# Performance work log

Measured on AMD Instinct MI355X. Metric: run time of the kernel, lower is better.

## Reference

```python
import jax, jax.numpy as jnp
import numpy as np

# Conv / geometry config (matches init_kwargs)
CIN, COUT = 16, 32
H, W = 16, 16
KH, KW = 3, 3
STRIDE, PAD = 1, 1
OH = (H + 2 * PAD - KH) // STRIDE + 1
OW = (W + 2 * PAD - KW) // STRIDE + 1
IN_DIM = CIN * H * W      # 4096
OUT_DIM = COUT * OH * OW  # 8192
N = 256                   # number of constraint rows


def full_toeplitz(weight):
    """Dense Toeplitz matrix T [Cout*Oh*Ow, Cin*H*W] with conv(x) = T @ x.flatten().

    out[co,oh,ow] = sum_{ci,kh,kw} w[co,ci,kh,kw] * x[ci, oh*s+kh-p, ow*s+kw-p].
    So T entry at (co,oh,ow),(ci,ih,iw) = w[co,ci, ih-(oh*s-p), iw-(ow*s-p)] if in-range.
    """
    dt = weight.dtype
    oh = jnp.arange(OH)
    ih = jnp.arange(H)
    kh = ih[None, :] - (oh[:, None] * STRIDE - PAD)          # [Oh, H]
    mh = ((kh >= 0) & (kh < KH)).astype(dt)
    khc = jnp.clip(kh, 0, KH - 1)
    ow = jnp.arange(OW)
    iw = jnp.arange(W)
    kw = iw[None, :] - (ow[:, None] * STRIDE - PAD)          # [Ow, W]
    mw = ((kw >= 0) & (kw < KW)).astype(dt)
    kwc = jnp.clip(kw, 0, KW - 1)
    # gather kernel rows: [Cout, Cin, Oh, H, Kw]
    g1 = weight[:, :, khc, :] * mh[None, None, :, :, None]
    # gather kernel cols: [Cout, Cin, Oh, H, Ow, W]
    g2 = g1[..., kwc] * mw[None, None, None, None, :, :]
    T = g2.transpose(0, 2, 4, 1, 3, 5).reshape(OUT_DIM, IN_DIM)
    return T


def setup_inputs() -> dict:
    key = jax.random.key(0)
    ks = jax.random.split(key, 6)
    return {
        "uc": jax.random.normal(ks[0], (N, OUT_DIM), dtype=jnp.float32),
        "lc": jax.random.normal(ks[1], (N, OUT_DIM), dtype=jnp.float32),
        "uc_bias": jax.random.normal(ks[2], (N,), dtype=jnp.float32),
        "lc_bias": jax.random.normal(ks[3], (N,), dtype=jnp.float32),
        "weight": jax.random.normal(ks[4], (COUT, CIN, KH, KW), dtype=jnp.float32),
        "bias": jax.random.normal(ks[5], (COUT,), dtype=jnp.float32),
    }


def reference(uc, lc, uc_bias, lc_bias, weight, bias):
    # VerifyConv2d._init_linear: Toeplitz weights + repeat_interleave'd bias,
    # then VerifyLinear.backsubstitute: dense GEMMs.
    T = full_toeplitz(weight)                      # [out_dim, in_dim]
    bvec = jnp.repeat(bias, OH * OW)               # [out_dim]
    new_uc_bias = uc_bias + uc @ bvec              # [N]
    new_lc_bias = lc_bias + lc @ bvec              # [N]
    new_uc = uc @ T                                # [N, in_dim]
    new_lc = lc @ T                                # [N, in_dim]
    return new_uc, new_lc, new_uc_bias, new_lc_bias
```

## Files before the change

kernel.cpp:

```cpp
#include <hip/hip_runtime.h>


#define NROWS   256
#define OUT_CH  32
#define IN_CH   16
#define SPAT    256
#define IN_DIM  4096
#define OUT_DIM 8192
#define CO_STRIDE 289

typedef __attribute__((ext_vector_type(8))) short    bf16x8;
typedef __attribute__((ext_vector_type(4))) float    f32x4;
typedef __attribute__((ext_vector_type(4))) unsigned u32x4;

__global__ __launch_bounds__(256) void backsub(
    const float* __restrict__ uc, const float* __restrict__ lc,
    const float* __restrict__ ucb, const float* __restrict__ lcb,
    const float* __restrict__ w, const float* __restrict__ bias,
    float* __restrict__ out)
{
    __shared__ float act[OUT_CH * CO_STRIDE];
    __shared__ unsigned short bfr16[9 * 2 * 512];
    __shared__ float red[4];

    const int t     = threadIdx.x;
    const int n     = blockIdx.x & 255;
    const int which = blockIdx.x >> 8;

    for (int i = t; i < OUT_CH * 16 * 2; i += 256) {
        int co = i >> 5, rr = i & 31, row = rr >> 1, side = rr & 1;
        act[co * CO_STRIDE + row * 18 + side * 17] = 0.f;
    }

    #pragma unroll
    for (int i = 0; i < 18; ++i) {
        int v = t + i * 256;
        int j = v >> 9, rem = v & 511, co = rem >> 4, ci = rem & 15;
        float wv = w[(co * IN_CH + ci) * 9 + j];
        unsigned hb = __float_as_uint(wv) & 0xffff0000u;
        float    lf = wv - __uint_as_float(hb);
        unsigned lb = __float_as_uint(lf) & 0xffff0000u;
        int lane = ((co >> 3) << 4) | ci;
        int r    = co & 7;
        bfr16[(2 * j + 0) * 512 + lane * 8 + r] = (unsigned short)(hb >> 16);
        bfr16[(2 * j + 1) * 512 + lane * 8 + r] = (unsigned short)(lb >> 16);
    }

    const float*  srow = (which ? lc : uc) + (size_t)n * OUT_DIM;
    const float4* s4   = (const float4*)srow;
    float bs = 0.f;
    #pragma unroll
    for (int k = 0; k < 8; ++k) {
        float4 f = s4[t + k * 256];
        int co  = (t >> 6) + 4 * k;
        bs += bias[co] * (f.x + f.y + f.z + f.w);
        int ih  = (t >> 2) & 15;
        int iw0 = (t & 3) * 4;
        int wd  = co * CO_STRIDE + ih * 18 + 1 + iw0;
        act[wd + 0] = f.x; act[wd + 1] = f.y; act[wd + 2] = f.z; act[wd + 3] = f.w;
    }
    #pragma unroll
    for (int o = 32; o > 0; o >>= 1) bs += __shfl_down(bs, o, 64);
    if ((t & 63) == 0) red[t >> 6] = bs;

    __syncthreads();

    if (t == 0) {
        const float* cb = which ? lcb : ucb;
        out[2 * (size_t)NROWS * IN_DIM + which * NROWS + n] =
            cb[n] + red[0] + red[1] + red[2] + red[3];
    }

    const int l    = t & 63;
    const int wave = t >> 6;
    const int co_g = l >> 4;
    const int il   = l & 15;

    bf16x8 Bh[9], Bl[9];
    #pragma unroll
    for (int j = 0; j < 9; ++j) {
        Bh[j] = *(const bf16x8*)&bfr16[(2 * j + 0) * 512 + l * 8];
        Bl[j] = *(const bf16x8*)&bfr16[(2 * j + 1) * 512 + l * 8];
    }

    f32x4 acc[4];
    #pragma unroll
    for (int mt = 0; mt < 4; ++mt) acc[mt] = (f32x4){0.f, 0.f, 0.f, 0.f};

    #pragma unroll
    for (int mt = 0; mt < 4; ++mt) {
        const int ih = wave * 4 + mt;
        #pragma unroll
        for (int j = 0; j < 9; ++j) {
            const int kh = j / 3, kw = j % 3;
            const int ihn = ih + 1 - kh;
            if ((unsigned)ihn < 16u) {
                const float* p = &act[co_g * (8 * CO_STRIDE) + ihn * 18 + il + 2 - kw];
                u32x4 hv, lv;
                #pragma unroll
                for (int q = 0; q < 4; ++q) {
                    float a0 = p[(2 * q)     * CO_STRIDE];
                    float a1 = p[(2 * q + 1) * CO_STRIDE];
                    unsigned h0 = __float_as_uint(a0) & 0xffff0000u;
                    unsigned h1 = __float_as_uint(a1) & 0xffff0000u;
                    float l0 = a0 - __uint_as_float(h0);
                    float l1 = a1 - __uint_as_float(h1);
                    hv[q] = (h0 >> 16) | h1;
                    lv[q] = (__float_as_uint(l0) >> 16)
                          | (__float_as_uint(l1) & 0xffff0000u);
                }
                bf16x8 ah = __builtin_bit_cast(bf16x8, hv);
                bf16x8 al = __builtin_bit_cast(bf16x8, lv);
                acc[mt] = __builtin_amdgcn_mfma_f32_16x16x32_bf16(ah, Bh[j], acc[mt], 0, 0, 0);
                acc[mt] = __builtin_amdgcn_mfma_f32_16x16x32_bf16(ah, Bl[j], acc[mt], 0, 0, 0);
                acc[mt] = __builtin_amdgcn_mfma_f32_16x16x32_bf16(al, Bh[j], acc[mt], 0, 0, 0);
            }
        }
        float* ob = out + (size_t)which * (NROWS * IN_DIM) + (size_t)n * IN_DIM
                  + il * SPAT + wave * 64 + mt * 16 + co_g * 4;
        *(f32x4*)ob = acc[mt];
    }
}

extern "C" void kernel_launch(void* const* d_in, const int* in_sizes, int n_in,
                              void* d_out, int out_size, void* d_ws, size_t ws_size,
                              hipStream_t stream) {
    const float* uc   = (const float*)d_in[0];
    const float* lc   = (const float*)d_in[1];
    const float* ucb  = (const float*)d_in[2];
    const float* lcb  = (const float*)d_in[3];
    const float* w    = (const float*)d_in[4];
    const float* bias = (const float*)d_in[5];

    backsub<<<512, 256, 0, stream>>>(uc, lc, ucb, lcb, w, bias, (float*)d_out);
}
```

Baseline: 86.96 us.

## Pre-split activations into packed bf16 hi/lo pairs in swizzled LDS layout

Activations are now converted to bf16 hi/lo pairs once, at staging time, and stored packed by channel pair in a padded, XOR-swizzled LDS layout. The MFMA loop can then fetch each A operand with two 128-bit LDS reads instead of eight scalar reads plus repeated split arithmetic for every kernel tap. Global loads are issued at the start of the kernel so they overlap the weight staging. The costs are a more complex indexing scheme and slightly more LDS.

Result: faster. 83.37 us (-4.1%).

```diff
diff --git a/kernel.cpp b/kernel.cpp
--- a/kernel.cpp
+++ b/kernel.cpp
@@ -7,7 +7,8 @@
 #define SPAT    256
 #define IN_DIM  4096
 #define OUT_DIM 8192
-#define CO_STRIDE 289
+#define PSTR    20
+#define PA_HALF (288 * PSTR)
 
 typedef __attribute__((ext_vector_type(8))) short    bf16x8;
 typedef __attribute__((ext_vector_type(4))) float    f32x4;
@@ -19,17 +20,24 @@
     const float* __restrict__ w, const float* __restrict__ bias,
     float* __restrict__ out)
 {
-    __shared__ float act[OUT_CH * CO_STRIDE];
+    __shared__ unsigned packA[2 * PA_HALF];
     __shared__ unsigned short bfr16[9 * 2 * 512];
     __shared__ float red[4];
 
     const int t     = threadIdx.x;
+    const int lane  = t & 63;
+    const int wave  = t >> 6;
     const int n     = blockIdx.x & 255;
     const int which = blockIdx.x >> 8;
 
-    for (int i = t; i < OUT_CH * 16 * 2; i += 256) {
-        int co = i >> 5, rr = i & 31, row = rr >> 1, side = rr & 1;
-        act[co * CO_STRIDE + row * 18 + side * 17] = 0.f;
+    const float*  srow = (which ? lc : uc) + (size_t)n * OUT_DIM;
+    const float4* s4   = (const float4*)srow;
+    float4 av[4], bv[4];
+    #pragma unroll
+    for (int k = 0; k < 4; ++k) {
+        int p = wave * 4 + k;
+        av[k] = s4[(2 * p) * 64 + lane];
+        bv[k] = s4[(2 * p + 1) * 64 + lane];
     }
 
     #pragma unroll
@@ -40,28 +48,46 @@
         unsigned hb = __float_as_uint(wv) & 0xffff0000u;
         float    lf = wv - __uint_as_float(hb);
         unsigned lb = __float_as_uint(lf) & 0xffff0000u;
-        int lane = ((co >> 3) << 4) | ci;
-        int r    = co & 7;
-        bfr16[(2 * j + 0) * 512 + lane * 8 + r] = (unsigned short)(hb >> 16);
-        bfr16[(2 * j + 1) * 512 + lane * 8 + r] = (unsigned short)(lb >> 16);
+        int bl = ((co >> 3) << 4) | ci;
+        int r  = co & 7;
+        bfr16[(2 * j + 0) * 512 + bl * 8 + r] = (unsigned short)(hb >> 16);
+        bfr16[(2 * j + 1) * 512 + bl * 8 + r] = (unsigned short)(lb >> 16);
     }
 
-    const float*  srow = (which ? lc : uc) + (size_t)n * OUT_DIM;
-    const float4* s4   = (const float4*)srow;
+    for (int i = t; i < 1024; i += 256) {
+        int p = i & 15, sp = (i >> 4) & 31, a = i >> 9;
+        int s = (sp >> 1) * 18 + (sp & 1) * 17;
+        packA[a * PA_HALF + s * PSTR + p] = 0u;
+    }
+
     float bs = 0.f;
+    const int row18 = lane >> 2;
+    const int iw0   = (lane & 3) * 4;
     #pragma unroll
-    for (int k = 0; k < 8; ++k) {
-        float4 f = s4[t + k * 256];
-        int co  = (t >> 6) + 4 * k;
-        bs += bias[co] * (f.x + f.y + f.z + f.w);
-        int ih  = (t >> 2) & 15;
-        int iw0 = (t & 3) * 4;
-        int wd  = co * CO_STRIDE + ih * 18 + 1 + iw0;
-        act[wd + 0] = f.x; act[wd + 1] = f.y; act[wd + 2] = f.z; act[wd + 3] = f.w;
+    for (int k = 0; k < 4; ++k) {
+        int p = wave * 4 + k;
+        float4 a = av[k], b = bv[k];
+        bs += bias[2 * p]     * (a.x + a.y + a.z + a.w);
+        bs += bias[2 * p + 1] * (b.x + b.y + b.z + b.w);
+        const float* ae = (const float*)&a;
+        const float* be = (const float*)&b;
+        int s0 = row18 * 18 + 1 + iw0;
+        #pragma unroll
+        for (int i = 0; i < 4; ++i) {
+            int s  = s0 + i;
+            int pw = p ^ (((s >> 3) & 3) << 2);
+            unsigned ha = __float_as_uint(ae[i]) & 0xffff0000u;
+            unsigned hb = __float_as_uint(be[i]) & 0xffff0000u;
+            float la = ae[i] - __uint_as_float(ha);
+            float lb = be[i] - __uint_as_float(hb);
+            packA[s * PSTR + pw] = (ha >> 16) | hb;
+            packA[PA_HALF + s * PSTR + pw] =
+                (__float_as_uint(la) >> 16) | (__float_as_uint(lb) & 0xffff0000u);
+        }
     }
     #pragma unroll
     for (int o = 32; o > 0; o >>= 1) bs += __shfl_down(bs, o, 64);
-    if ((t & 63) == 0) red[t >> 6] = bs;
+    if ((t & 63) == 0) red[wave] = bs;
 
     __syncthreads();
 
@@ -71,16 +97,13 @@
             cb[n] + red[0] + red[1] + red[2] + red[3];
     }
 
-    const int l    = t & 63;
-    const int wave = t >> 6;
-    const int co_g = l >> 4;
-    const int il   = l & 15;
-
+    const int cg = lane >> 4;
+    const int il = lane & 15;
     bf16x8 Bh[9], Bl[9];
     #pragma unroll
     for (int j = 0; j < 9; ++j) {
-        Bh[j] = *(const bf16x8*)&bfr16[(2 * j + 0) * 512 + l * 8];
-        Bl[j] = *(const bf16x8*)&bfr16[(2 * j + 1) * 512 + l * 8];
+        Bh[j] = *(const bf16x8*)&bfr16[(2 * j + 0) * 512 + lane * 8];
+        Bl[j] = *(const bf16x8*)&bfr16[(2 * j + 1) * 512 + lane * 8];
     }
 
     f32x4 acc[4];
@@ -95,20 +118,11 @@
             const int kh = j / 3, kw = j % 3;
             const int ihn = ih + 1 - kh;
             if ((unsigned)ihn < 16u) {
-                const float* p = &act[co_g * (8 * CO_STRIDE) + ihn * 18 + il + 2 - kw];
-                u32x4 hv, lv;
-                #pragma unroll
-                for (int q = 0; q < 4; ++q) {
-                    float a0 = p[(2 * q)     * CO_STRIDE];
-                    float a1 = p[(2 * q + 1) * CO_STRIDE];
-                    unsigned h0 = __float_as_uint(a0) & 0xffff0000u;
-                    unsigned h1 = __float_as_uint(a1) & 0xffff0000u;
-                    float l0 = a0 - __uint_as_float(h0);
-                    float l1 = a1 - __uint_as_float(h1);
-                    hv[q] = (h0 >> 16) | h1;
-                    lv[q] = (__float_as_uint(l0) >> 16)
-                          | (__float_as_uint(l1) & 0xffff0000u);
-                }
+                int s    = ihn * 18 + il + 2 - kw;
+                int cgx  = cg ^ ((s >> 3) & 3);
+                int word = s * PSTR + cgx * 4;
+                u32x4 hv = *(const u32x4*)&packA[word];
+                u32x4 lv = *(const u32x4*)&packA[PA_HALF + word];
                 bf16x8 ah = __builtin_bit_cast(bf16x8, hv);
                 bf16x8 al = __builtin_bit_cast(bf16x8, lv);
                 acc[mt] = __builtin_amdgcn_mfma_f32_16x16x32_bf16(ah, Bh[j], acc[mt], 0, 0, 0);
@@ -117,7 +131,7 @@
             }
         }
         float* ob = out + (size_t)which * (NROWS * IN_DIM) + (size_t)n * IN_DIM
-                  + il * SPAT + wave * 64 + mt * 16 + co_g * 4;
+                  + il * SPAT + wave * 64 + mt * 16 + cg * 4;
         *(f32x4*)ob = acc[mt];
     }
 }
```
